# Optimization experiments

Measured on AMD Instinct MI355X. Metric: run time of the kernel, lower is better.

The kernel has to match this reference:

```python
import jax, jax.numpy as jnp
import numpy as np

B, T, D = 2, 1024, 2048
H, KV, Dh = 16, 4, 128
REP = H // KV
LAMBDA_INIT = 0.8 - 0.6 * float(np.exp(-0.3 * 0))  # depth=0 -> 0.2
ROPE_THETA = 10000.0


def rope_cos_sin(pos, dh):
    # standard rotary embedding tables, half-split (rotate_half) convention
    inv_freq = 1.0 / (ROPE_THETA ** (jnp.arange(0, dh, 2, dtype=jnp.float32) / dh))
    freqs = pos.astype(jnp.float32)[:, None] * inv_freq[None, :]  # (T, Dh/2)
    return jnp.cos(freqs), jnp.sin(freqs)


def apply_rope(x, cos, sin):
    # x: (B, H, T, Dh); cos/sin: (T, Dh/2)
    x1, x2 = jnp.split(x, 2, axis=-1)
    c = cos[None, None, :, :]
    s = sin[None, None, :, :]
    return jnp.concatenate([x1 * c - x2 * s, x1 * s + x2 * c], axis=-1)


def setup_inputs() -> dict:
    key = jax.random.key(0)
    ks = jax.random.split(key, 5)
    std = 0.02
    return {
        "x": jax.random.normal(ks[0], (B, T, D), dtype=jnp.float32),
        "wq": jax.random.normal(ks[1], (D, 2 * H * Dh), dtype=jnp.float32) * std,
        "wk": jax.random.normal(ks[2], (D, 2 * KV * Dh), dtype=jnp.float32) * std,
        "wv": jax.random.normal(ks[3], (D, 2 * KV * Dh), dtype=jnp.float32) * std,
        "wo": jax.random.normal(ks[4], (2 * H * Dh, D), dtype=jnp.float32) * std,
    }


def reference(x, wq, wk, wv, wo):
    # projections (no bias)
    q = (x @ wq).reshape(B, T, H, 2 * Dh).transpose(0, 2, 1, 3)    # (B,H,T,2Dh)
    k = (x @ wk).reshape(B, T, KV, 2 * Dh).transpose(0, 2, 1, 3)   # (B,KV,T,2Dh)
    v = (x @ wv).reshape(B, T, KV, 2 * Dh).transpose(0, 2, 1, 3)   # (B,KV,T,2Dh)

    q1, q2 = jnp.split(q, 2, axis=-1)
    k1, k2 = jnp.split(k, 2, axis=-1)

    pos = jnp.arange(T)
    cos, sin = rope_cos_sin(pos, Dh)
    q1 = apply_rope(q1, cos, sin)
    q2 = apply_rope(q2, cos, sin)
    k1 = apply_rope(k1, cos, sin)
    k2 = apply_rope(k2, cos, sin)

    # GQA: repeat kv heads contiguously (matches expand+reshape)
    k1f = jnp.repeat(k1, REP, axis=1)
    k2f = jnp.repeat(k2, REP, axis=1)
    vf = jnp.repeat(v, REP, axis=1)  # (B,H,T,2Dh)

    scale = 1.0 / jnp.sqrt(jnp.float32(Dh))
    scores1 = jnp.einsum("bhtd,bhsd->bhts", q1, k1f) * scale
    scores2 = jnp.einsum("bhtd,bhsd->bhts", q2, k2f) * scale

    causal = jnp.triu(jnp.ones((T, T), dtype=bool), k=1)  # True above diagonal
    neg_inf = jnp.float32(-jnp.inf)
    scores1 = jnp.where(causal[None, None], neg_inf, scores1)
    scores2 = jnp.where(causal[None, None], neg_inf, scores2)

    attn1 = jax.nn.softmax(scores1, axis=-1)
    attn2 = jax.nn.softmax(scores2, axis=-1)
    attn_diff = attn1 - LAMBDA_INIT * attn2

    out = jnp.einsum("bhts,bhsd->bhtd", attn_diff, vf)  # (B,H,T,2Dh)
    out = out.transpose(0, 2, 1, 3).reshape(B, T, 2 * H * Dh)
    return out @ wo  # (B,T,D)
```

## Files before the change

### kernel.cpp

```cpp
#include <hip/hip_runtime.h>
#include <hip/hip_bf16.h>
#include <stdint.h>

typedef __bf16 bf16_t;
typedef __attribute__((ext_vector_type(8))) __bf16 bf16x8;
typedef __attribute__((ext_vector_type(4))) __bf16 bf16x4;
typedef __attribute__((ext_vector_type(4))) float f32x4;

#define AS1 __attribute__((address_space(1)))
#define AS3 __attribute__((address_space(3)))

__device__ inline void gload_lds16(const void* g, void* l) {
    __builtin_amdgcn_global_load_lds((AS1 void*)(uintptr_t)g, (AS3 void*)l, 16, 0, 0);
}

__device__ inline f32x4 mfma_bf16_16x16x32(bf16x8 a, bf16x8 b, f32x4 c) {
    return __builtin_amdgcn_mfma_f32_16x16x32_bf16(a, b, c, 0, 0, 0);
}


__global__ __launch_bounds__(256) void cast_x_kernel(const float* __restrict__ x,
                                                     bf16_t* __restrict__ xb, int n) {
    int i = (blockIdx.x * 256 + threadIdx.x) * 4;
    if (i >= n) return;
    float4 v = *reinterpret_cast<const float4*>(x + i);
    bf16x4 o;
    o[0] = (bf16_t)v.x; o[1] = (bf16_t)v.y; o[2] = (bf16_t)v.z; o[3] = (bf16_t)v.w;
    *reinterpret_cast<bf16x4*>(xb + i) = o;
}

__global__ __launch_bounds__(256) void transpose_cast_w(const float* __restrict__ s0,
                                                        const float* __restrict__ s1,
                                                        const float* __restrict__ s2,
                                                        int n1, int n2,
                                                        int ld0, int ld1, int ld2,
                                                        int K, int N, bf16_t* __restrict__ dst) {
    __shared__ float tile[32][33];
    const int kt = blockIdx.x * 32, nt = blockIdx.y * 32;
    const int tx = threadIdx.x & 31, ty = threadIdx.x >> 5;
    #pragma unroll
    for (int j = 0; j < 4; j++) {
        int k = kt + ty + j * 8;
        int n = nt + tx;
        float v;
        if (n < n1)      v = s0[(size_t)k * ld0 + n];
        else if (n < n2) v = s1[(size_t)k * ld1 + (n - n1)];
        else             v = s2[(size_t)k * ld2 + (n - n2)];
        tile[ty + j * 8][tx] = v;
    }
    __syncthreads();
    #pragma unroll
    for (int j = 0; j < 4; j++) {
        int n = nt + ty + j * 8;
        int k = kt + tx;
        dst[(size_t)n * K + k] = (bf16_t)tile[tx][ty + j * 8];
    }
}

__global__ __launch_bounds__(256) void rope_qk(bf16_t* __restrict__ qkv) {
    int tid = blockIdx.x * 256 + threadIdx.x;
    int i = tid & 63;
    int u = (tid >> 6) % 40;
    int row = tid / 2560;
    int base;
    if (u < 32) base = (u >> 1) * 256 + (u & 1) * 128;
    else { int uu = u - 32; base = 4096 + (uu >> 1) * 256 + (uu & 1) * 128; }
    bf16_t* p = qkv + (size_t)row * 6144 + base;
    float x1 = (float)p[i];
    float x2 = (float)p[i + 64];
    int t = row & 1023;
    float invf = exp2f(-0.20762050593045893f * (float)i);
    float a = (float)t * invf;
    float c = cosf(a), s = sinf(a);
    p[i]      = (bf16_t)(x1 * c - x2 * s);
    p[i + 64] = (bf16_t)(x1 * s + x2 * c);
}

__global__ __launch_bounds__(256) void pack_vt(const bf16_t* __restrict__ qkv,
                                               bf16_t* __restrict__ vt) {
    __shared__ bf16_t tile[32][33];
    const int st = blockIdx.x * 32, dt = blockIdx.y * 32, bkv = blockIdx.z;
    const int b = bkv >> 2, kv = bkv & 3;
    const int tx = threadIdx.x & 31, ty = threadIdx.x >> 5;
    #pragma unroll
    for (int j = 0; j < 4; j++) {
        int s = st + ty + j * 8;
        tile[ty + j * 8][tx] = qkv[(size_t)(b * 1024 + s) * 6144 + 5120 + kv * 256 + dt + tx];
    }
    __syncthreads();
    #pragma unroll
    for (int j = 0; j < 4; j++) {
        int d = dt + ty + j * 8;
        vt[(size_t)(bkv * 256 + d) * 1024 + st + tx] = tile[tx][ty + j * 8];
    }
}

template <int BN, int OUT_BF16>
__global__ __launch_bounds__(256, 3) void gemm_bt(const bf16_t* __restrict__ A,
                                                  const bf16_t* __restrict__ Bt,
                                                  void* __restrict__ Cv,
                                                  int M, int N, int K) {
    constexpr int ASZ = 128 * 32;
    constexpr int BSZ = BN * 32;
    constexpr int MI = (BN == 128) ? 4 : 2;
    __shared__ bf16_t As[2 * ASZ];
    __shared__ bf16_t Bs[2 * BSZ];
    const int tid = threadIdx.x;
    const int w = tid >> 6, l = tid & 63;
    const int lq = l & 15, g = l >> 4;
    const int wrow = (BN == 128) ? ((w >> 1) * 64) : (w * 32);
    const int wcol = (BN == 128) ? ((w & 1) * 64) : 0;
    const size_t m0 = (size_t)blockIdx.x * 128;
    const size_t n0 = (size_t)blockIdx.y * BN;
    f32x4 acc[MI][4];
    #pragma unroll
    for (int i = 0; i < MI; i++)
        #pragma unroll
        for (int j = 0; j < 4; j++) { acc[i][j][0] = 0.f; acc[i][j][1] = 0.f; acc[i][j][2] = 0.f; acc[i][j][3] = 0.f; }
    const int rowi = l >> 2;
    const int ko = (l & 3) * 8;
    const bf16_t* Ab = A + (m0 + rowi) * K + ko;
    const bf16_t* Bb = Bt + (n0 + rowi) * K + ko;
    const int nt = K / 32;

    auto stage = [&](int buf, int t) {
        const int k0 = t * 32;
        #pragma unroll
        for (int j = 0; j < 2; j++) {
            const int c = j * 4 + w;
            gload_lds16(Ab + (size_t)(c * 16) * K + k0, As + buf * ASZ + c * 512);
        }
        if constexpr (BN == 128) {
            #pragma unroll
            for (int j = 0; j < 2; j++) {
                const int c = j * 4 + w;
                gload_lds16(Bb + (size_t)(c * 16) * K + k0, Bs + buf * BSZ + c * 512);
            }
        } else {
            gload_lds16(Bb + (size_t)(w * 16) * K + k0, Bs + buf * BSZ + w * 512);
        }
    };

    stage(0, 0);
    __syncthreads();
    int cur = 0;
    for (int t = 0; t < nt; t++) {
        if (t + 1 < nt) stage(cur ^ 1, t + 1);
        bf16x8 af[MI], bfv[4];
        #pragma unroll
        for (int mi = 0; mi < MI; mi++)
            af[mi] = *reinterpret_cast<const bf16x8*>(&As[cur * ASZ + (wrow + mi * 16 + lq) * 32 + g * 8]);
        #pragma unroll
        for (int ni = 0; ni < 4; ni++)
            bfv[ni] = *reinterpret_cast<const bf16x8*>(&Bs[cur * BSZ + (wcol + ni * 16 + lq) * 32 + g * 8]);
        #pragma unroll
        for (int mi = 0; mi < MI; mi++)
            #pragma unroll
            for (int ni = 0; ni < 4; ni++)
                acc[mi][ni] = mfma_bf16_16x16x32(af[mi], bfv[ni], acc[mi][ni]);
        __syncthreads();
        cur ^= 1;
    }
    #pragma unroll
    for (int mi = 0; mi < MI; mi++)
        #pragma unroll
        for (int ni = 0; ni < 4; ni++)
            #pragma unroll
            for (int r = 0; r < 4; r++) {
                size_t row = m0 + wrow + mi * 16 + 4 * g + r;
                size_t col = n0 + wcol + ni * 16 + lq;
                float v = acc[mi][ni][r];
                if (OUT_BF16) ((bf16_t*)Cv)[row * N + col] = (bf16_t)v;
                else          ((float*)Cv)[row * N + col] = v;
            }
}

__global__ __launch_bounds__(256, 3) void attn_fused(const bf16_t* __restrict__ qkv,
                                                     const bf16_t* __restrict__ vt,
                                                     bf16_t* __restrict__ ao) {
    const int bh = blockIdx.x;
    const int y = blockIdx.y;
    const int qt = (y < 8) ? 31 - y : (y < 16) ? y + 8 : (y < 24) ? 31 - y : y - 24;
    const int b = bh >> 4, h = bh & 15, kv = h >> 2;
    const int tid = threadIdx.x;
    const int w = tid >> 6, l = tid & 63;
    const int rg = w >> 1, wh = w & 1;
    const int lq = l & 15, g = l >> 4;
    const int q0 = qt * 32;
    const float scale = 0.08838834764831845f;

    __shared__ char smem[16384 + 16384 + 4 * 1280];
    bf16_t* Ks  = (bf16_t*)smem;
    bf16_t* Vs  = (bf16_t*)(smem + 16384);
    bf16_t* Ps  = (bf16_t*)(smem + 32768) + w * 640;
    bf16_t* O2s = (bf16_t*)smem;

    bf16x8 qf[4];
    {
        const bf16_t* qp = qkv + (size_t)(b * 1024 + q0 + rg * 16 + lq) * 6144 + h * 256 + wh * 128 + g * 8;
        #pragma unroll
        for (int c = 0; c < 4; c++) qf[c] = *reinterpret_cast<const bf16x8*>(qp + c * 32);
    }
    const int t = q0 + rg * 16 + lq;

    const int kr_off = l >> 5;
    const int kc16   = l & 31;
    const int vd_off = l >> 2;
    const int vc16   = l & 3;

    const bf16_t* kgbase = qkv + (size_t)(b * 1024) * 6144 + 4096 + kv * 256;
    const bf16_t* vgbase = vt + (size_t)((b * 4 + kv) * 256) * 1024;

    float m = -1e30f, lsum = 0.f;
    f32x4 oacc[16];
    #pragma unroll
    for (int dt = 0; dt < 16; dt++) { oacc[dt][0] = 0.f; oacc[dt][1] = 0.f; oacc[dt][2] = 0.f; oacc[dt][3] = 0.f; }

    const int nr = qt + 1;
    for (int rnd = 0; rnd < nr; ++rnd) {
        const int s0 = rnd * 32;
        #pragma unroll
        for (int j = 0; j < 4; j++) {
            int r = 8 * w + 2 * j + kr_off;
            int d = (kc16 ^ (r & 7)) * 8;
            gload_lds16(kgbase + (size_t)(s0 + r) * 6144 + d, Ks + (8 * w + 2 * j) * 256);
        }
        #pragma unroll
        for (int j = 0; j < 4; j++) {
            int d = 64 * w + 16 * j + vd_off;
            int sc = (vc16 ^ ((d >> 1) & 3)) * 8;
            gload_lds16(vgbase + (size_t)d * 1024 + s0 + sc, Vs + (64 * w + 16 * j) * 32);
        }
        __syncthreads();

        f32x4 stA, stB;
        stA[0] = stA[1] = stA[2] = stA[3] = 0.f;
        stB[0] = stB[1] = stB[2] = stB[3] = 0.f;
        #pragma unroll
        for (int c = 0; c < 4; c++) {
            const int c16 = wh * 16 + c * 4 + g;
            const int rA = lq, rB = 16 + lq;
            bf16x8 kfa = *reinterpret_cast<const bf16x8*>(Ks + rA * 256 + ((c16 ^ (rA & 7)) * 8));
            bf16x8 kfb = *reinterpret_cast<const bf16x8*>(Ks + rB * 256 + ((c16 ^ (rB & 7)) * 8));
            stA = mfma_bf16_16x16x32(kfa, qf[c], stA);
            stB = mfma_bf16_16x16x32(kfb, qf[c], stB);
        }
        const bool lastr = (rnd == nr - 1);
        float pA[4], pB[4];
        float tmax = -1e30f;
        #pragma unroll
        for (int r = 0; r < 4; r++) {
            float a  = stA[r] * scale;
            float bv = stB[r] * scale;
            if (lastr) {
                if (s0 + 4 * g + r > t)      a  = -1e30f;
                if (s0 + 16 + 4 * g + r > t) bv = -1e30f;
            }
            pA[r] = a; pB[r] = bv;
            tmax = fmaxf(tmax, fmaxf(a, bv));
        }
        tmax = fmaxf(tmax, __shfl_xor(tmax, 16));
        tmax = fmaxf(tmax, __shfl_xor(tmax, 32));
        if (__any(tmax > m + 8.f)) {
            const float mnew = fmaxf(m, tmax);
            const float alpha = __expf(m - mnew);
            m = mnew;
            lsum *= alpha;
            float al[4];
            #pragma unroll
            for (int r = 0; r < 4; r++) al[r] = __shfl(alpha, 4 * g + r);
            #pragma unroll
            for (int dt = 0; dt < 16; dt++) {
                oacc[dt][0] *= al[0]; oacc[dt][1] *= al[1]; oacc[dt][2] *= al[2]; oacc[dt][3] *= al[3];
            }
        }
        float ps = 0.f;
        #pragma unroll
        for (int r = 0; r < 4; r++) {
            pA[r] = __expf(pA[r] - m);
            pB[r] = __expf(pB[r] - m);
            ps += pA[r] + pB[r];
        }
        ps += __shfl_xor(ps, 16);
        ps += __shfl_xor(ps, 32);
        lsum += ps;
        bf16x4 wa, wb;
        #pragma unroll
        for (int r = 0; r < 4; r++) { wa[r] = (bf16_t)pA[r]; wb[r] = (bf16_t)pB[r]; }
        *reinterpret_cast<bf16x4*>(&Ps[lq * 40 + 4 * g]) = wa;
        *reinterpret_cast<bf16x4*>(&Ps[lq * 40 + 16 + 4 * g]) = wb;
        bf16x8 pf = *reinterpret_cast<const bf16x8*>(&Ps[lq * 40 + 8 * g]);
        #pragma unroll
        for (int dt = 0; dt < 16; dt++) {
            const int d = dt * 16 + lq;
            bf16x8 vf = *reinterpret_cast<const bf16x8*>(Vs + d * 32 + ((g ^ ((d >> 1) & 3)) * 8));
            oacc[dt] = mfma_bf16_16x16x32(pf, vf, oacc[dt]);
        }
        __syncthreads();
    }

    float li[4];
    #pragma unroll
    for (int r = 0; r < 4; r++) li[r] = 1.0f / __shfl(lsum, 4 * g + r);

    if (wh == 1) {
        #pragma unroll
        for (int dt = 0; dt < 16; dt++)
            #pragma unroll
            for (int r = 0; r < 4; r++)
                O2s[(rg * 16 + 4 * g + r) * 256 + dt * 16 + lq] = (bf16_t)(oacc[dt][r] * li[r]);
    }
    __syncthreads();
    if (wh == 0) {
        #pragma unroll
        for (int dt = 0; dt < 16; dt++)
            #pragma unroll
            for (int r = 0; r < 4; r++) {
                const int qloc = rg * 16 + 4 * g + r;
                float o2 = (float)O2s[qloc * 256 + dt * 16 + lq];
                ao[(size_t)(b * 1024 + q0 + qloc) * 4096 + h * 256 + dt * 16 + lq] =
                    (bf16_t)(oacc[dt][r] * li[r] - 0.2f * o2);
            }
    }
}


extern "C" void kernel_launch(void* const* d_in, const int* in_sizes, int n_in,
                              void* d_out, int out_size, void* d_ws, size_t ws_size,
                              hipStream_t stream) {
    (void)in_sizes; (void)n_in; (void)out_size;
    const float* x  = (const float*)d_in[0];
    const float* wq = (const float*)d_in[1];
    const float* wk = (const float*)d_in[2];
    const float* wv = (const float*)d_in[3];
    const float* wo = (const float*)d_in[4];

    char* ws = (char*)d_ws;
    size_t off = 0;
    auto alloc = [&](size_t bytes) {
        void* p = ws + off;
        off += (bytes + 255) & ~(size_t)255;
        return p;
    };
    bf16_t* xb   = (bf16_t*)alloc(4194304ull * 2);
    bf16_t* wbt  = (bf16_t*)alloc(6144ull * 2048 * 2);
    bf16_t* wot  = (bf16_t*)alloc(2048ull * 4096 * 2);
    bf16_t* qkvb = (bf16_t*)alloc(2048ull * 6144 * 2);
    bf16_t* vtb  = (bf16_t*)alloc(8ull * 256 * 1024 * 2);
    bf16_t* ao   = (bf16_t*)alloc(2048ull * 4096 * 2);
    if (off > ws_size) return;

    cast_x_kernel<<<4096, 256, 0, stream>>>(x, xb, 4194304);
    transpose_cast_w<<<dim3(64, 192), 256, 0, stream>>>(wq, wk, wv, 4096, 5120,
                                                        4096, 1024, 1024, 2048, 6144, wbt);
    transpose_cast_w<<<dim3(128, 64), 256, 0, stream>>>(wo, wo, wo, 1 << 28, 1 << 28,
                                                        2048, 2048, 2048, 4096, 2048, wot);
    gemm_bt<128, 1><<<dim3(16, 48), 256, 0, stream>>>(xb, wbt, qkvb, 2048, 6144, 2048);
    rope_qk<<<20480, 256, 0, stream>>>(qkvb);
    pack_vt<<<dim3(32, 8, 8), 256, 0, stream>>>(qkvb, vtb);
    attn_fused<<<dim3(32, 32), 256, 0, stream>>>(qkvb, vtb, ao);
    gemm_bt<64, 0><<<dim3(16, 32), 256, 0, stream>>>(ao, wot, (float*)d_out, 2048, 2048, 4096);
}
```

Before: 236.6 us.

## Double-buffer K tiles, read V from global, swizzle grids for XCD locality

The attention kernel now double-buffers K tiles in LDS, prefetching the next tile while the current one is computed, and reads V fragments straight from global memory instead of staging them in LDS. It also raises the occupancy hint to 4 and wraps the MFMA sections in s_setprio. Both GEMMs and the attention kernel now launch 1D grids with an XCD-aware block swizzle, so neighbouring tiles land on the same chiplet and share L2. Reading V directly from global may increase latency stalls, and the attention work order changes from the previous mixed heavy/light query-tile schedule to a heaviest-first order.

Result: slower. 427.7 us (+80.8%).

```diff
diff --git a/kernel.cpp b/kernel.cpp
--- a/kernel.cpp
+++ b/kernel.cpp
@@ -110,8 +110,11 @@
     const int lq = l & 15, g = l >> 4;
     const int wrow = (BN == 128) ? ((w >> 1) * 64) : (w * 32);
     const int wcol = (BN == 128) ? ((w & 1) * 64) : 0;
-    const size_t m0 = (size_t)blockIdx.x * 128;
-    const size_t n0 = (size_t)blockIdx.y * BN;
+    const int lin = blockIdx.x;
+    const int chunk = gridDim.x >> 3;
+    const int swz = (lin & 7) * chunk + (lin >> 3);
+    const size_t m0 = (size_t)(swz & 15) * 128;
+    const size_t n0 = (size_t)(swz >> 4) * BN;
     f32x4 acc[MI][4];
     #pragma unroll
     for (int i = 0; i < MI; i++)
@@ -175,12 +178,13 @@
             }
 }
 
-__global__ __launch_bounds__(256, 3) void attn_fused(const bf16_t* __restrict__ qkv,
+__global__ __launch_bounds__(256, 4) void attn_fused(const bf16_t* __restrict__ qkv,
                                                      const bf16_t* __restrict__ vt,
                                                      bf16_t* __restrict__ ao) {
-    const int bh = blockIdx.x;
-    const int y = blockIdx.y;
-    const int qt = (y < 8) ? 31 - y : (y < 16) ? y + 8 : (y < 24) ? 31 - y : y - 24;
+    const int lin = blockIdx.x;
+    const int logical = (lin & 7) * 128 + (lin >> 3);
+    const int bh = logical >> 5;
+    const int qt = 31 - (logical & 31);
     const int b = bh >> 4, h = bh & 15, kv = h >> 2;
     const int tid = threadIdx.x;
     const int w = tid >> 6, l = tid & 63;
@@ -189,9 +193,8 @@
     const int q0 = qt * 32;
     const float scale = 0.08838834764831845f;
 
-    __shared__ char smem[16384 + 16384 + 4 * 1280];
+    __shared__ char smem[2 * 16384 + 4 * 1280];
     bf16_t* Ks  = (bf16_t*)smem;
-    bf16_t* Vs  = (bf16_t*)(smem + 16384);
     bf16_t* Ps  = (bf16_t*)(smem + 32768) + w * 640;
     bf16_t* O2s = (bf16_t*)smem;
 
@@ -205,46 +208,47 @@
 
     const int kr_off = l >> 5;
     const int kc16   = l & 31;
-    const int vd_off = l >> 2;
-    const int vc16   = l & 3;
 
     const bf16_t* kgbase = qkv + (size_t)(b * 1024) * 6144 + 4096 + kv * 256;
     const bf16_t* vgbase = vt + (size_t)((b * 4 + kv) * 256) * 1024;
 
-    float m = -1e30f, lsum = 0.f;
-    f32x4 oacc[16];
-    #pragma unroll
-    for (int dt = 0; dt < 16; dt++) { oacc[dt][0] = 0.f; oacc[dt][1] = 0.f; oacc[dt][2] = 0.f; oacc[dt][3] = 0.f; }
-
-    const int nr = qt + 1;
-    for (int rnd = 0; rnd < nr; ++rnd) {
-        const int s0 = rnd * 32;
+    auto stageK = [&](int buf, int s0) {
         #pragma unroll
         for (int j = 0; j < 4; j++) {
             int r = 8 * w + 2 * j + kr_off;
             int d = (kc16 ^ (r & 7)) * 8;
-            gload_lds16(kgbase + (size_t)(s0 + r) * 6144 + d, Ks + (8 * w + 2 * j) * 256);
-        }
-        #pragma unroll
-        for (int j = 0; j < 4; j++) {
-            int d = 64 * w + 16 * j + vd_off;
-            int sc = (vc16 ^ ((d >> 1) & 3)) * 8;
-            gload_lds16(vgbase + (size_t)d * 1024 + s0 + sc, Vs + (64 * w + 16 * j) * 32);
-        }
-        __syncthreads();
-
+            gload_lds16(kgbase + (size_t)(s0 + r) * 6144 + d, Ks + buf * 8192 + (8 * w + 2 * j) * 256);
+        }
+    };
+
+    float m = -1e30f, lsum = 0.f;
+    f32x4 oacc[16];
+    #pragma unroll
+    for (int dt = 0; dt < 16; dt++) { oacc[dt][0] = 0.f; oacc[dt][1] = 0.f; oacc[dt][2] = 0.f; oacc[dt][3] = 0.f; }
+
+    const int nr = qt + 1;
+    stageK(0, 0);
+    __syncthreads();
+    int cur = 0;
+    for (int rnd = 0; rnd < nr; ++rnd) {
+        const int s0 = rnd * 32;
+        if (rnd + 1 < nr) stageK(cur ^ 1, s0 + 32);
+
+        const bf16_t* Kc = Ks + cur * 8192;
         f32x4 stA, stB;
         stA[0] = stA[1] = stA[2] = stA[3] = 0.f;
         stB[0] = stB[1] = stB[2] = stB[3] = 0.f;
+        __builtin_amdgcn_s_setprio(1);
         #pragma unroll
         for (int c = 0; c < 4; c++) {
             const int c16 = wh * 16 + c * 4 + g;
             const int rA = lq, rB = 16 + lq;
-            bf16x8 kfa = *reinterpret_cast<const bf16x8*>(Ks + rA * 256 + ((c16 ^ (rA & 7)) * 8));
-            bf16x8 kfb = *reinterpret_cast<const bf16x8*>(Ks + rB * 256 + ((c16 ^ (rB & 7)) * 8));
+            bf16x8 kfa = *reinterpret_cast<const bf16x8*>(Kc + rA * 256 + ((c16 ^ (rA & 7)) * 8));
+            bf16x8 kfb = *reinterpret_cast<const bf16x8*>(Kc + rB * 256 + ((c16 ^ (rB & 7)) * 8));
             stA = mfma_bf16_16x16x32(kfa, qf[c], stA);
             stB = mfma_bf16_16x16x32(kfb, qf[c], stB);
         }
+        __builtin_amdgcn_s_setprio(0);
         const bool lastr = (rnd == nr - 1);
         float pA[4], pB[4];
         float tmax = -1e30f;
@@ -290,13 +294,16 @@
         *reinterpret_cast<bf16x4*>(&Ps[lq * 40 + 4 * g]) = wa;
         *reinterpret_cast<bf16x4*>(&Ps[lq * 40 + 16 + 4 * g]) = wb;
         bf16x8 pf = *reinterpret_cast<const bf16x8*>(&Ps[lq * 40 + 8 * g]);
+        __builtin_amdgcn_s_setprio(1);
         #pragma unroll
         for (int dt = 0; dt < 16; dt++) {
             const int d = dt * 16 + lq;
-            bf16x8 vf = *reinterpret_cast<const bf16x8*>(Vs + d * 32 + ((g ^ ((d >> 1) & 3)) * 8));
+            bf16x8 vf = *reinterpret_cast<const bf16x8*>(vgbase + (size_t)d * 1024 + s0 + 8 * g);
             oacc[dt] = mfma_bf16_16x16x32(pf, vf, oacc[dt]);
         }
+        __builtin_amdgcn_s_setprio(0);
         __syncthreads();
+        cur ^= 1;
     }
 
     float li[4];
@@ -355,9 +362,9 @@
                                                         4096, 1024, 1024, 2048, 6144, wbt);
     transpose_cast_w<<<dim3(128, 64), 256, 0, stream>>>(wo, wo, wo, 1 << 28, 1 << 28,
                                                         2048, 2048, 2048, 4096, 2048, wot);
-    gemm_bt<128, 1><<<dim3(16, 48), 256, 0, stream>>>(xb, wbt, qkvb, 2048, 6144, 2048);
+    gemm_bt<128, 1><<<768, 256, 0, stream>>>(xb, wbt, qkvb, 2048, 6144, 2048);
     rope_qk<<<20480, 256, 0, stream>>>(qkvb);
     pack_vt<<<dim3(32, 8, 8), 256, 0, stream>>>(qkvb, vtb);
-    attn_fused<<<dim3(32, 32), 256, 0, stream>>>(qkvb, vtb, ao);
-    gemm_bt<64, 0><<<dim3(16, 32), 256, 0, stream>>>(ao, wot, (float*)d_out, 2048, 2048, 4096);
-}
+    attn_fused<<<1024, 256, 0, stream>>>(qkvb, vtb, ao);
+    gemm_bt<64, 0><<<512, 256, 0, stream>>>(ao, wot, (float*)d_out, 2048, 2048, 4096);
+}
```
